# Kernel tuning notes

Hardware: AMD Instinct MI355X
Metric: run time of the kernel (lower is better)

Reference implementation:

```python
import jax, jax.numpy as jnp
import numpy as np

B, N, F, H, N_ITERS = 64, 256, 16, 256, 10


def setup_inputs() -> dict:
    key = jax.random.key(0)
    ks = jax.random.split(key, 20)
    s = 0.05
    jets = jax.random.normal(ks[0], (B, N, F), dtype=jnp.float32)
    # row-normalized dense adjacency (D^-1 A style)
    a = jax.random.uniform(ks[1], (B, N, N), dtype=jnp.float32)
    dads = a / jnp.sum(a, axis=-1, keepdims=True)
    p = lambda k, sh: jax.random.normal(k, sh, dtype=jnp.float32) * s
    return {
        'jets': jets, 'dads': dads,
        'W_emb': p(ks[2], (F, H)), 'b_emb': jnp.zeros((H,), jnp.float32),
        'W_msg': p(ks[3], (H, H)), 'b_msg': jnp.zeros((H,), jnp.float32),
        # GRU vertex update: input = concat(message[H], s[F]) -> H
        'Wz': p(ks[4], (H + F, H)), 'Uz': p(ks[5], (H, H)), 'bz': jnp.zeros((H,), jnp.float32),
        'Wr': p(ks[6], (H + F, H)), 'Ur': p(ks[7], (H, H)), 'br': jnp.zeros((H,), jnp.float32),
        'Wh': p(ks[8], (H + F, H)), 'Uh': p(ks[9], (H, H)), 'bh': jnp.zeros((H,), jnp.float32),
        'W_r1': p(ks[10], (H, H)), 'b_r1': jnp.zeros((H,), jnp.float32),
        'W_r2': p(ks[11], (H, H)), 'b_r2': jnp.zeros((H,), jnp.float32),
    }


def reference(jets, dads, W_emb, b_emb, W_msg, b_msg,
              Wz, Uz, bz, Wr, Ur, br, Wh, Uh, bh,
              W_r1, b_r1, W_r2, b_r2):
    # Embedding: [B,N,F] -> [B,N,H]
    h = jnp.tanh(jets @ W_emb + b_emb)
    for _ in range(N_ITERS):
        # Message: linear then adjacency aggregation + tanh
        m = jnp.tanh(jnp.matmul(dads, h @ W_msg + b_msg))  # [B,N,H]
        # GRU-style vertex update; input = concat(message, original features s)
        x = jnp.concatenate([m, jets], axis=-1)            # [B,N,H+F]
        z = jax.nn.sigmoid(x @ Wz + h @ Uz + bz)
        r = jax.nn.sigmoid(x @ Wr + h @ Ur + br)
        h_tilde = jnp.tanh(x @ Wh + (r * h) @ Uh + bh)
        h = (1.0 - z) * h + z * h_tilde
    # Readout: per-node MLP then sum over nodes -> [B,H]
    out = jnp.sum(jnp.tanh(h @ W_r1 + b_r1) @ W_r2 + b_r2, axis=1)
    return out
```

## Files before the change

kernel.cpp:

```cpp
#include <hip/hip_runtime.h>

#define DEVI __device__ __forceinline__

typedef __attribute__((ext_vector_type(4))) float f32x4;
typedef __attribute__((ext_vector_type(8))) short s16x8;
typedef __attribute__((ext_vector_type(4))) short s16x4;
typedef unsigned short u16;
typedef unsigned int u32;

#define WST 288
#define SROW 264
#define AST 260

DEVI u16 f2bf(float x){
  u32 u = __float_as_uint(x);
  u = (u + 0x7fffu + ((u >> 16) & 1u)) >> 16;
  return (u16)u;
}
DEVI float bf2f(u16 v){ return __uint_as_float(((u32)v) << 16); }

DEVI float fsigm(float x){ return __builtin_amdgcn_rcpf(1.f + __builtin_amdgcn_exp2f(-1.442695041f * x)); }
DEVI float ftanh(float x){ float e = __builtin_amdgcn_exp2f(2.885390082f * x); return 1.f - 2.f * __builtin_amdgcn_rcpf(e + 1.f); }

DEVI s16x8 ld8(const u16* p){ return *(const s16x8*)p; }
DEVI s16x8 ldb64p(const u16* p){
  s16x4 lo = *(const s16x4*)p;
  s16x4 hi = *(const s16x4*)(p + 4);
  s16x8 r;
  r[0]=lo[0]; r[1]=lo[1]; r[2]=lo[2]; r[3]=lo[3];
  r[4]=hi[0]; r[5]=hi[1]; r[6]=hi[2]; r[7]=hi[3];
  return r;
}

DEVI f32x4 ld4bf(const u16* p){
  uint2 v = *(const uint2*)p;
  f32x4 r;
  r[0] = bf2f((u16)(v.x & 0xffff)); r[1] = bf2f((u16)(v.x >> 16));
  r[2] = bf2f((u16)(v.y & 0xffff)); r[3] = bf2f((u16)(v.y >> 16));
  return r;
}

DEVI void st4bf(u16* p, float a, float b, float c, float d){
  uint2 v;
  v.x = (u32)f2bf(a) | ((u32)f2bf(b) << 16);
  v.y = (u32)f2bf(c) | ((u32)f2bf(d) << 16);
  *(uint2*)p = v;
}

#define MFMA(a,b,c) __builtin_amdgcn_mfma_f32_16x16x32_bf16((a),(b),(c),0,0,0)

__global__ void k_prep(
  const float* __restrict__ jets, const float* __restrict__ dads, const float* __restrict__ W_emb,
  const float* __restrict__ W_msg, const float* __restrict__ Wz, const float* __restrict__ Uz,
  const float* __restrict__ Wr, const float* __restrict__ Ur, const float* __restrict__ Wh,
  const float* __restrict__ Uh, const float* __restrict__ W_r1,
  u16* __restrict__ jp, u16* __restrict__ dadsb, u16* __restrict__ Wet, u16* __restrict__ Wmt,
  u16* __restrict__ Wzt, u16* __restrict__ Uzt, u16* __restrict__ Wrt, u16* __restrict__ Urt,
  u16* __restrict__ Wht, u16* __restrict__ Uht, u16* __restrict__ Wr1t)
{
  int blk = blockIdx.x, tid = threadIdx.x;
  if(blk < 1280){
    int mi = blk >> 8, k = blk & 255, j = tid;
    const float* src; u16* dst;
    switch(mi){
      case 0: src = W_msg; dst = Wmt;  break;
      case 1: src = Uz;    dst = Uzt;  break;
      case 2: src = Ur;    dst = Urt;  break;
      case 3: src = Uh;    dst = Uht;  break;
      default: src = W_r1; dst = Wr1t; break;
    }
    dst[j*256 + k] = f2bf(src[k*256 + j]);
  } else if(blk < 2144){
    int q = blk - 1280; int mi = q / 288; int k = q - mi*288; int j = tid;
    const float* src; u16* dst;
    switch(mi){ case 0: src = Wz; dst = Wzt; break; case 1: src = Wr; dst = Wrt; break; default: src = Wh; dst = Wht; break; }
    dst[j*WST + k] = (k < 272) ? f2bf(src[k*256 + j]) : (u16)0;
  } else if(blk < 2176){
    int idx = (blk - 2144)*256 + tid;
    int j = idx >> 5, k = idx & 31;
    Wet[idx] = (k < 16) ? f2bf(W_emb[k*256 + j]) : (u16)0;
  } else if(blk < 4224){
    int idx = (blk - 2176)*256 + tid;
    int n = idx >> 5, k = idx & 31;
    jp[idx] = (k < 16) ? f2bf(jets[n*16 + k]) : (u16)0;
  } else {
    int idx = (blk - 4224)*256 + tid;
    f32x4 v = *(const f32x4*)(dads + (size_t)idx*4);
    st4bf(dadsb + (size_t)idx*4, v[0], v[1], v[2], v[3]);
  }
}

__global__ __launch_bounds__(256,3) void k_embed(
  u16* __restrict__ h, u16* __restrict__ hmo,
  const u16* __restrict__ jp, const u16* __restrict__ Wet, const float* __restrict__ be,
  const u16* __restrict__ Wmt, const float* __restrict__ bm)
{
  __shared__ u16 hbuf[16*SROW];
  const int tid = threadIdx.x;
  const int wv = tid >> 6, lane = tid & 63, ln = lane & 15, qd = lane >> 4;
  const int n0 = blockIdx.x * 16;
  const int b  = n0 >> 8;
  const int nb = n0 & 255;
  const int nodeA = n0 + ln;

  s16x8 jfr = ld8(jp + (size_t)nodeA*32 + qd*8);
#pragma unroll
  for(int t = 0; t < 4; t++){
    int j0 = (wv*4 + t) * 16;
    f32x4 acc = {0.f,0.f,0.f,0.f};
    s16x8 a = ld8(Wet + (size_t)(j0 + ln)*32 + qd*8);
    acc = MFMA(a, jfr, acc);
    f32x4 bv = *(const f32x4*)(be + j0 + qd*4);
    f32x4 hv;
#pragma unroll
    for(int r = 0; r < 4; r++) hv[r] = ftanh(acc[r] + bv[r]);
    st4bf(h + (size_t)nodeA*256 + j0 + qd*4, hv[0], hv[1], hv[2], hv[3]);
    st4bf(&hbuf[ln*SROW + j0 + qd*4], hv[0], hv[1], hv[2], hv[3]);
  }
  __syncthreads();

  s16x8 af[8];
#pragma unroll
  for(int c = 0; c < 8; c++) af[c] = ld8(&hbuf[ln*SROW + c*32 + qd*8]);
#pragma unroll
  for(int tp = 0; tp < 2; tp++){
    int j0 = (wv*4 + tp*2) * 16, j1 = j0 + 16;
    f32x4 a0 = {0.f,0.f,0.f,0.f}, a1 = {0.f,0.f,0.f,0.f};
#pragma unroll
    for(int c = 0; c < 8; c++){
      a0 = MFMA(af[c], ld8(Wmt + (size_t)(j0 + ln)*256 + c*32 + qd*8), a0);
      a1 = MFMA(af[c], ld8(Wmt + (size_t)(j1 + ln)*256 + c*32 + qd*8), a1);
    }
    float b0 = bm[j0 + ln], b1 = bm[j1 + ln];
    st4bf(hmo + (size_t)(b*256 + j0 + ln)*256 + nb + qd*4, a0[0]+b0, a0[1]+b0, a0[2]+b0, a0[3]+b0);
    st4bf(hmo + (size_t)(b*256 + j1 + ln)*256 + nb + qd*4, a1[0]+b1, a1[1]+b1, a1[2]+b1, a1[3]+b1);
  }
}

__global__ __launch_bounds__(256,1) void k_gru(
  u16* __restrict__ h,
  const u16* __restrict__ hmi, u16* __restrict__ hmo,
  const u16* __restrict__ dadsb, const u16* __restrict__ jp,
  const u16* __restrict__ Wzt, const u16* __restrict__ Wrt, const u16* __restrict__ Wht,
  const u16* __restrict__ Uzt, const u16* __restrict__ Urt, const u16* __restrict__ Uht,
  const u16* __restrict__ Wmt,
  const float* __restrict__ bz, const float* __restrict__ br, const float* __restrict__ bhb,
  const float* __restrict__ bm)
{
  __shared__ u16 smM[64*AST];
  __shared__ u16 smB[64*AST];
  const int tid = threadIdx.x;
  const int wv = tid >> 6, lane = tid & 63, ln = lane & 15, qd = lane >> 4;
  const int blk   = blockIdx.x;
  const int batch = (blk & 7) * 8 + (blk >> 5);
  const int group = (blk >> 3) & 3;
  const int n0 = batch * 256 + group * 64;
  const int b  = batch;
  const int nb = group * 64;
  const int j0w = wv * 64;

  const u16* Ab1 = hmi + (size_t)(b*256 + j0w + ln)*256 + qd*8;
  s16x8 Am[3][4];
#pragma unroll
  for(int p = 0; p < 2; p++)
#pragma unroll
    for(int t = 0; t < 4; t++)
      Am[p][t] = ld8(Ab1 + (size_t)t*16*256 + p*32);

  s16x8 jB[4];
#pragma unroll
  for(int i = 0; i < 4; i++) jB[i] = ld8(jp + (size_t)(n0 + i*16 + ln)*32 + qd*8);

  {
    f32x4 acc[4][4];
#pragma unroll
    for(int t = 0; t < 4; t++)
#pragma unroll
      for(int i = 0; i < 4; i++) acc[t][i] = (f32x4){0.f,0.f,0.f,0.f};
    s16x8 Bf[4], Bn[4];
#pragma unroll
    for(int i = 0; i < 4; i++) Bf[i] = ld8(dadsb + (size_t)(n0 + i*16 + ln)*256 + qd*8);
#pragma unroll
    for(int c = 0; c < 8; c++){
      if(c < 6){
#pragma unroll
        for(int t = 0; t < 4; t++) Am[(c+2)%3][t] = ld8(Ab1 + (size_t)t*16*256 + (c+2)*32);
      }
      if(c < 7){
#pragma unroll
        for(int i = 0; i < 4; i++) Bn[i] = ld8(dadsb + (size_t)(n0 + i*16 + ln)*256 + (c+1)*32 + qd*8);
      }
#pragma unroll
      for(int t = 0; t < 4; t++){
        s16x8 A = Am[c%3][t];
#pragma unroll
        for(int i = 0; i < 4; i++) acc[t][i] = MFMA(A, Bf[i], acc[t][i]);
      }
      if(c < 7){
#pragma unroll
        for(int i = 0; i < 4; i++) Bf[i] = Bn[i];
      }
    }
#pragma unroll
    for(int t = 0; t < 4; t++)
#pragma unroll
      for(int i = 0; i < 4; i++)
        st4bf(&smM[(i*16 + ln)*AST + j0w + t*16 + qd*4],
              ftanh(acc[t][i][0]), ftanh(acc[t][i][1]), ftanh(acc[t][i][2]), ftanh(acc[t][i][3]));
  }
  const u16* AbWr = Wrt + (size_t)(j0w + ln)*WST + qd*8;
  const u16* AbUr = Urt + (size_t)(j0w + ln)*256 + qd*8;
  s16x8 RW[3][4], RU[3][4];
#pragma unroll
  for(int p = 0; p < 2; p++)
#pragma unroll
    for(int t = 0; t < 4; t++){
      RW[p][t] = ld8(AbWr + (size_t)t*16*WST + p*32);
      RU[p][t] = ld8(AbUr + (size_t)t*16*256 + p*32);
    }
  __syncthreads();

  {
    f32x4 acc[4][4];
#pragma unroll
    for(int t = 0; t < 4; t++)
#pragma unroll
      for(int i = 0; i < 4; i++) acc[t][i] = (f32x4){0.f,0.f,0.f,0.f};
    s16x8 Ajr[4];
#pragma unroll
    for(int t = 0; t < 4; t++) Ajr[t] = ld8(AbWr + (size_t)t*16*WST + 256);
    s16x8 Bh[4], Bn[4];
#pragma unroll
    for(int i = 0; i < 4; i++) Bh[i] = ld8(h + (size_t)(n0 + i*16 + ln)*256 + qd*8);
#pragma unroll
    for(int c = 0; c < 8; c++){
      if(c < 6){
#pragma unroll
        for(int t = 0; t < 4; t++){
          RW[(c+2)%3][t] = ld8(AbWr + (size_t)t*16*WST + (c+2)*32);
          RU[(c+2)%3][t] = ld8(AbUr + (size_t)t*16*256 + (c+2)*32);
        }
      }
      if(c < 7){
#pragma unroll
        for(int i = 0; i < 4; i++) Bn[i] = ld8(h + (size_t)(n0 + i*16 + ln)*256 + (c+1)*32 + qd*8);
      }
      s16x8 Bm[4];
#pragma unroll
      for(int i = 0; i < 4; i++) Bm[i] = ldb64p(&smM[(i*16 + ln)*AST + c*32 + qd*8]);
#pragma unroll
      for(int t = 0; t < 4; t++){
        s16x8 Aw = RW[c%3][t];
#pragma unroll
        for(int i = 0; i < 4; i++) acc[t][i] = MFMA(Aw, Bm[i], acc[t][i]);
      }
#pragma unroll
      for(int t = 0; t < 4; t++){
        s16x8 Au = RU[c%3][t];
#pragma unroll
        for(int i = 0; i < 4; i++) acc[t][i] = MFMA(Au, Bh[i], acc[t][i]);
      }
      if(c < 7){
#pragma unroll
        for(int i = 0; i < 4; i++) Bh[i] = Bn[i];
      }
    }
#pragma unroll
    for(int t = 0; t < 4; t++)
#pragma unroll
      for(int i = 0; i < 4; i++) acc[t][i] = MFMA(Ajr[t], jB[i], acc[t][i]);
#pragma unroll
    for(int t = 0; t < 4; t++){
      f32x4 bv = *(const f32x4*)(br + j0w + t*16 + qd*4);
#pragma unroll
      for(int i = 0; i < 4; i++){
        f32x4 hv = ld4bf(h + (size_t)(n0 + i*16 + ln)*256 + j0w + t*16 + qd*4);
        st4bf(&smB[(i*16 + ln)*AST + j0w + t*16 + qd*4],
              fsigm(acc[t][i][0]+bv[0])*hv[0], fsigm(acc[t][i][1]+bv[1])*hv[1],
              fsigm(acc[t][i][2]+bv[2])*hv[2], fsigm(acc[t][i][3]+bv[3])*hv[3]);
      }
    }
  }
  const u16* AbWz = Wzt + (size_t)(j0w + ln)*WST + qd*8;
  const u16* AbUz = Uzt + (size_t)(j0w + ln)*256 + qd*8;
  s16x8 ZW[3][4], ZU[3][4];
#pragma unroll
  for(int p = 0; p < 2; p++)
#pragma unroll
    for(int t = 0; t < 4; t++){
      ZW[p][t] = ld8(AbWz + (size_t)t*16*WST + p*32);
      ZU[p][t] = ld8(AbUz + (size_t)t*16*256 + p*32);
    }
  __syncthreads();

  f32x4 zacc[4][4], gacc[4][4];
#pragma unroll
  for(int t = 0; t < 4; t++)
#pragma unroll
    for(int i = 0; i < 4; i++) zacc[t][i] = (f32x4){0.f,0.f,0.f,0.f};
  {
    s16x8 Ajz[4];
#pragma unroll
    for(int t = 0; t < 4; t++) Ajz[t] = ld8(AbWz + (size_t)t*16*WST + 256);
    s16x8 Bh[4], Bn[4];
#pragma unroll
    for(int i = 0; i < 4; i++) Bh[i] = ld8(h + (size_t)(n0 + i*16 + ln)*256 + qd*8);
#pragma unroll
    for(int c = 0; c < 8; c++){
      if(c < 6){
#pragma unroll
        for(int t = 0; t < 4; t++){
          ZW[(c+2)%3][t] = ld8(AbWz + (size_t)t*16*WST + (c+2)*32);
          ZU[(c+2)%3][t] = ld8(AbUz + (size_t)t*16*256 + (c+2)*32);
        }
      }
      if(c < 7){
#pragma unroll
        for(int i = 0; i < 4; i++) Bn[i] = ld8(h + (size_t)(n0 + i*16 + ln)*256 + (c+1)*32 + qd*8);
      }
      s16x8 Bm[4];
#pragma unroll
      for(int i = 0; i < 4; i++) Bm[i] = ldb64p(&smM[(i*16 + ln)*AST + c*32 + qd*8]);
#pragma unroll
      for(int t = 0; t < 4; t++){
        s16x8 Aw = ZW[c%3][t];
#pragma unroll
        for(int i = 0; i < 4; i++) zacc[t][i] = MFMA(Aw, Bm[i], zacc[t][i]);
      }
#pragma unroll
      for(int t = 0; t < 4; t++){
        s16x8 Au = ZU[c%3][t];
#pragma unroll
        for(int i = 0; i < 4; i++) zacc[t][i] = MFMA(Au, Bh[i], zacc[t][i]);
      }
      if(c < 7){
#pragma unroll
        for(int i = 0; i < 4; i++) Bh[i] = Bn[i];
      }
    }
#pragma unroll
    for(int t = 0; t < 4; t++)
#pragma unroll
      for(int i = 0; i < 4; i++) zacc[t][i] = MFMA(Ajz[t], jB[i], zacc[t][i]);
  }

  const u16* AbWh = Wht + (size_t)(j0w + ln)*WST + qd*8;
  const u16* AbUh = Uht + (size_t)(j0w + ln)*256 + qd*8;
  s16x8 GW[3][4], GU[3][4];
#pragma unroll
  for(int p = 0; p < 2; p++)
#pragma unroll
    for(int t = 0; t < 4; t++){
      GW[p][t] = ld8(AbWh + (size_t)t*16*WST + p*32);
      GU[p][t] = ld8(AbUh + (size_t)t*16*256 + p*32);
    }

#pragma unroll
  for(int t = 0; t < 4; t++)
#pragma unroll
    for(int i = 0; i < 4; i++) gacc[t][i] = (f32x4){0.f,0.f,0.f,0.f};
  {
    s16x8 Ajh[4];
#pragma unroll
    for(int t = 0; t < 4; t++) Ajh[t] = ld8(AbWh + (size_t)t*16*WST + 256);
#pragma unroll
    for(int c = 0; c < 8; c++){
      if(c < 6){
#pragma unroll
        for(int t = 0; t < 4; t++){
          GW[(c+2)%3][t] = ld8(AbWh + (size_t)t*16*WST + (c+2)*32);
          GU[(c+2)%3][t] = ld8(AbUh + (size_t)t*16*256 + (c+2)*32);
        }
      }
      s16x8 Bm[4], Brh[4];
#pragma unroll
      for(int i = 0; i < 4; i++){
        Bm[i]  = ldb64p(&smM[(i*16 + ln)*AST + c*32 + qd*8]);
        Brh[i] = ldb64p(&smB[(i*16 + ln)*AST + c*32 + qd*8]);
      }
#pragma unroll
      for(int t = 0; t < 4; t++){
        s16x8 Aw = GW[c%3][t];
#pragma unroll
        for(int i = 0; i < 4; i++) gacc[t][i] = MFMA(Aw, Bm[i], gacc[t][i]);
      }
#pragma unroll
      for(int t = 0; t < 4; t++){
        s16x8 Au = GU[c%3][t];
#pragma unroll
        for(int i = 0; i < 4; i++) gacc[t][i] = MFMA(Au, Brh[i], gacc[t][i]);
      }
    }
#pragma unroll
    for(int t = 0; t < 4; t++)
#pragma unroll
      for(int i = 0; i < 4; i++) gacc[t][i] = MFMA(Ajh[t], jB[i], gacc[t][i]);
  }
  __syncthreads();

#pragma unroll
  for(int t = 0; t < 4; t++){
    f32x4 bzv = *(const f32x4*)(bz + j0w + t*16 + qd*4);
    f32x4 bhv = *(const f32x4*)(bhb + j0w + t*16 + qd*4);
#pragma unroll
    for(int i = 0; i < 4; i++){
      f32x4 hv = ld4bf(h + (size_t)(n0 + i*16 + ln)*256 + j0w + t*16 + qd*4);
      f32x4 hn;
#pragma unroll
      for(int r = 0; r < 4; r++){
        float z  = fsigm(zacc[t][i][r] + bzv[r]);
        float th = ftanh(gacc[t][i][r] + bhv[r]);
        hn[r] = hv[r] + z * (th - hv[r]);
      }
      st4bf(h + (size_t)(n0 + i*16 + ln)*256 + j0w + t*16 + qd*4, hn[0], hn[1], hn[2], hn[3]);
      st4bf(&smM[(i*16 + ln)*AST + j0w + t*16 + qd*4], hn[0], hn[1], hn[2], hn[3]);
    }
  }
  const u16* AbWm = Wmt + (size_t)(j0w + ln)*256 + qd*8;
  s16x8 MW[3][4];
#pragma unroll
  for(int p = 0; p < 2; p++)
#pragma unroll
    for(int t = 0; t < 4; t++)
      MW[p][t] = ld8(AbWm + (size_t)t*16*256 + p*32);
  __syncthreads();

  {
    f32x4 acc[4][4];
#pragma unroll
    for(int t = 0; t < 4; t++)
#pragma unroll
      for(int i = 0; i < 4; i++) acc[t][i] = (f32x4){0.f,0.f,0.f,0.f};
#pragma unroll
    for(int c = 0; c < 8; c++){
      if(c < 6){
#pragma unroll
        for(int t = 0; t < 4; t++) MW[(c+2)%3][t] = ld8(AbWm + (size_t)t*16*256 + (c+2)*32);
      }
      s16x8 Bf[4];
#pragma unroll
      for(int i = 0; i < 4; i++) Bf[i] = ldb64p(&smM[(i*16 + ln)*AST + c*32 + qd*8]);
#pragma unroll
      for(int t = 0; t < 4; t++){
        s16x8 A = MW[c%3][t];
#pragma unroll
        for(int i = 0; i < 4; i++) acc[t][i] = MFMA(A, Bf[i], acc[t][i]);
      }
    }
#pragma unroll
    for(int t = 0; t < 4; t++){
      f32x4 bmv = *(const f32x4*)(bm + j0w + t*16 + qd*4);
#pragma unroll
      for(int i = 0; i < 4; i++){
#pragma unroll
        for(int r = 0; r < 4; r++){
          hmo[(size_t)(b*256 + j0w + t*16 + qd*4 + r)*256 + nb + i*16 + ln] =
            f2bf(acc[t][i][r] + bmv[r]);
        }
      }
    }
  }
}

__global__ __launch_bounds__(256,3) void k_t(
  const u16* __restrict__ h, u16* __restrict__ t_out,
  const u16* __restrict__ Wr1t, const float* __restrict__ br1)
{
  const int tid = threadIdx.x;
  const int wv = tid >> 6, lane = tid & 63, ln = lane & 15, qd = lane >> 4;
  const int n0 = blockIdx.x * 16;
  const int nodeA = n0 + ln;

  s16x8 hfr[8];
#pragma unroll
  for(int c = 0; c < 8; c++) hfr[c] = ld8(h + (size_t)nodeA*256 + c*32 + qd*8);
#pragma unroll
  for(int tp = 0; tp < 2; tp++){
    int j0 = (wv*4 + tp*2) * 16, j1 = j0 + 16;
    f32x4 a0 = {0.f,0.f,0.f,0.f}, a1 = {0.f,0.f,0.f,0.f};
#pragma unroll
    for(int c = 0; c < 8; c++){
      a0 = MFMA(ld8(Wr1t + (size_t)(j0 + ln)*256 + c*32 + qd*8), hfr[c], a0);
      a1 = MFMA(ld8(Wr1t + (size_t)(j1 + ln)*256 + c*32 + qd*8), hfr[c], a1);
    }
    f32x4 b0 = *(const f32x4*)(br1 + j0 + qd*4);
    f32x4 b1 = *(const f32x4*)(br1 + j1 + qd*4);
    st4bf(t_out + (size_t)nodeA*256 + j0 + qd*4,
          ftanh(a0[0]+b0[0]), ftanh(a0[1]+b0[1]), ftanh(a0[2]+b0[2]), ftanh(a0[3]+b0[3]));
    st4bf(t_out + (size_t)nodeA*256 + j1 + qd*4,
          ftanh(a1[0]+b1[0]), ftanh(a1[1]+b1[1]), ftanh(a1[2]+b1[2]), ftanh(a1[3]+b1[3]));
  }
}

__global__ void k_red(const u16* __restrict__ t, const float* __restrict__ W_r2,
                      const float* __restrict__ b_r2, float* __restrict__ out){
  __shared__ float s[256];
  int b = blockIdx.x, k = threadIdx.x;
  float acc = 0.f;
  for(int n = 0; n < 256; n++) acc += bf2f(t[(size_t)(b*256 + n)*256 + k]);
  s[k] = acc;
  __syncthreads();
  int j = threadIdx.x;
  float o = 256.f * b_r2[j];
  for(int k2 = 0; k2 < 256; k2++) o += s[k2] * W_r2[k2*256 + j];
  out[b*256 + j] = o;
}

extern "C" void kernel_launch(void* const* d_in, const int* in_sizes, int n_in,
                              void* d_out, int out_size, void* d_ws, size_t ws_size,
                              hipStream_t stream)
{
  const float* jets  = (const float*)d_in[0];
  const float* dads  = (const float*)d_in[1];
  const float* W_emb = (const float*)d_in[2];
  const float* b_emb = (const float*)d_in[3];
  const float* W_msg = (const float*)d_in[4];
  const float* b_msg = (const float*)d_in[5];
  const float* Wz    = (const float*)d_in[6];
  const float* Uz    = (const float*)d_in[7];
  const float* bz    = (const float*)d_in[8];
  const float* Wr    = (const float*)d_in[9];
  const float* Ur    = (const float*)d_in[10];
  const float* br    = (const float*)d_in[11];
  const float* Wh    = (const float*)d_in[12];
  const float* Uh    = (const float*)d_in[13];
  const float* bh    = (const float*)d_in[14];
  const float* W_r1  = (const float*)d_in[15];
  const float* b_r1  = (const float*)d_in[16];
  const float* W_r2  = (const float*)d_in[17];
  const float* b_r2  = (const float*)d_in[18];

  char* ws = (char*)d_ws;
  u16* h      = (u16*)(ws);
  u16* hmA    = (u16*)(ws + 8388608);
  u16* hmB    = (u16*)(ws + 16777216);
  u16* dadsb  = (u16*)(ws + 25165824);
  u16* jp     = (u16*)(ws + 33554432);
  u16* Wmt    = (u16*)(ws + 34603008);
  u16* Uzt    = (u16*)(ws + 34734080);
  u16* Urt    = (u16*)(ws + 34865152);
  u16* Uht    = (u16*)(ws + 34996224);
  u16* Wr1t   = (u16*)(ws + 35127296);
  u16* Wzt    = (u16*)(ws + 35258368);
  u16* Wrt    = (u16*)(ws + 35405824);
  u16* Wht    = (u16*)(ws + 35553280);
  u16* Wet    = (u16*)(ws + 35700736);
  float* outp = (float*)d_out;

  k_prep<<<8320, 256, 0, stream>>>(jets, dads, W_emb, W_msg, Wz, Uz, Wr, Ur, Wh, Uh, W_r1,
                                   jp, dadsb, Wet, Wmt, Wzt, Uzt, Wrt, Urt, Wht, Uht, Wr1t);
  k_embed<<<1024, 256, 0, stream>>>(h, hmA, jp, Wet, b_emb, Wmt, b_msg);
  for(int it = 0; it < 10; ++it){
    const u16* hin = (it & 1) ? hmB : hmA;
    u16* hout      = (it & 1) ? hmA : hmB;
    k_gru<<<256, 256, 0, stream>>>(h, hin, hout, dadsb, jp,
                                   Wzt, Wrt, Wht, Uzt, Urt, Uht, Wmt,
                                   bz, br, bh, b_msg);
  }
  k_t<<<1024, 256, 0, stream>>>(h, hmB, Wr1t, b_r1);
  k_red<<<64, 256, 0, stream>>>(hmB, W_r2, b_r2, outp);
}
```

Measured before the change: 644.2 us.

## Fuse GRU iterations into persistent cooperative kernel with LDS-resident hidden state

```diff
diff --git a/kernel.cpp b/kernel.cpp
--- a/kernel.cpp
+++ b/kernel.cpp
@@ -1,4 +1,7 @@
 #include <hip/hip_runtime.h>
+#include <hip/hip_cooperative_groups.h>
+
+namespace cg = cooperative_groups;
 
 #define DEVI __device__ __forceinline__
 
@@ -11,6 +14,8 @@
 #define WST 288
 #define SROW 264
 #define AST 260
+
+#define WAITVM(n) __builtin_amdgcn_s_waitcnt(((n)&0xF) | 0x70 | 0xF00 | (((n)>>4)<<14))
 
 DEVI u16 f2bf(float x){
   u32 u = __float_as_uint(x);
@@ -48,6 +53,17 @@
 }
 
 #define MFMA(a,b,c) __builtin_amdgcn_mfma_f32_16x16x32_bf16((a),(b),(c),0,0,0)
+
+DEVI void dma4(const u16* lanebase, int rowStrideElems, int c, u16* ldsbase){
+#pragma unroll
+  for(int q = 0; q < 4; q++){
+    const u16* g = lanebase + (size_t)q*16*rowStrideElems + c*32;
+    __builtin_amdgcn_global_load_lds((__attribute__((address_space(1))) const void*)g,
+                                     (__attribute__((address_space(3))) void*)(ldsbase + q*512),
+                                     16, 0, 0);
+  }
+}
+#define AFRAG(buf, t) ld8(&(buf)[(t)*512 + ln*32 + ((qd ^ ((ln>>1)&3))*8)])
 
 __global__ void k_prep(
   const float* __restrict__ jets, const float* __restrict__ dads, const float* __restrict__ W_emb,
@@ -149,6 +165,7 @@
 {
   __shared__ u16 smM[64*AST];
   __shared__ u16 smB[64*AST];
+  __shared__ __align__(16) u16 stg[4][2][2][2048];
   const int tid = threadIdx.x;
   const int wv = tid >> 6, lane = tid & 63, ln = lane & 15, qd = lane >> 4;
   const int blk   = blockIdx.x;
@@ -159,13 +176,16 @@
   const int nb = group * 64;
   const int j0w = wv * 64;
 
-  const u16* Ab1 = hmi + (size_t)(b*256 + j0w + ln)*256 + qd*8;
-  s16x8 Am[3][4];
-#pragma unroll
-  for(int p = 0; p < 2; p++)
-#pragma unroll
-    for(int t = 0; t < 4; t++)
-      Am[p][t] = ld8(Ab1 + (size_t)t*16*256 + p*32);
+  u16* s0 = &stg[wv][0][0][0];
+  u16* s1 = &stg[wv][1][0][0];
+  u16* u0 = &stg[wv][0][1][0];
+  u16* u1 = &stg[wv][1][1][0];
+
+  const int rw = lane >> 2;
+  const int cs = ((lane & 3) ^ ((lane >> 3) & 3)) * 8;
+
+  const u16* laneA = hmi + (size_t)(b*256 + j0w + rw)*256 + cs;
+  dma4(laneA, 256, 0, s0);
 
   s16x8 jB[4];
 #pragma unroll
@@ -182,17 +202,18 @@
     for(int i = 0; i < 4; i++) Bf[i] = ld8(dadsb + (size_t)(n0 + i*16 + ln)*256 + qd*8);
 #pragma unroll
     for(int c = 0; c < 8; c++){
-      if(c < 6){
-#pragma unroll
-        for(int t = 0; t < 4; t++) Am[(c+2)%3][t] = ld8(Ab1 + (size_t)t*16*256 + (c+2)*32);
-      }
+      u16* cur = (c & 1) ? s1 : s0;
       if(c < 7){
+        dma4(laneA, 256, c+1, (c & 1) ? s0 : s1);
 #pragma unroll
         for(int i = 0; i < 4; i++) Bn[i] = ld8(dadsb + (size_t)(n0 + i*16 + ln)*256 + (c+1)*32 + qd*8);
-      }
-#pragma unroll
-      for(int t = 0; t < 4; t++){
-        s16x8 A = Am[c%3][t];
+        WAITVM(8);
+      } else {
+        WAITVM(0);
+      }
+#pragma unroll
+      for(int t = 0; t < 4; t++){
+        s16x8 A = AFRAG(cur, t);
 #pragma unroll
         for(int i = 0; i < 4; i++) acc[t][i] = MFMA(A, Bf[i], acc[t][i]);
       }
@@ -208,16 +229,10 @@
         st4bf(&smM[(i*16 + ln)*AST + j0w + t*16 + qd*4],
               ftanh(acc[t][i][0]), ftanh(acc[t][i][1]), ftanh(acc[t][i][2]), ftanh(acc[t][i][3]));
   }
-  const u16* AbWr = Wrt + (size_t)(j0w + ln)*WST + qd*8;
-  const u16* AbUr = Urt + (size_t)(j0w + ln)*256 + qd*8;
-  s16x8 RW[3][4], RU[3][4];
-#pragma unroll
-  for(int p = 0; p < 2; p++)
-#pragma unroll
-    for(int t = 0; t < 4; t++){
-      RW[p][t] = ld8(AbWr + (size_t)t*16*WST + p*32);
-      RU[p][t] = ld8(AbUr + (size_t)t*16*256 + p*32);
-    }
+  const u16* laneWr = Wrt + (size_t)(j0w + rw)*WST + cs;
+  const u16* laneUr = Urt + (size_t)(j0w + rw)*256 + cs;
+  dma4(laneWr, WST, 0, s0);
+  dma4(laneUr, 256, 0, u0);
   __syncthreads();
 
   {
@@ -226,37 +241,37 @@
     for(int t = 0; t < 4; t++)
 #pragma unroll
       for(int i = 0; i < 4; i++) acc[t][i] = (f32x4){0.f,0.f,0.f,0.f};
-    s16x8 Ajr[4];
-#pragma unroll
-    for(int t = 0; t < 4; t++) Ajr[t] = ld8(AbWr + (size_t)t*16*WST + 256);
+    s16x8 Aj[4];
+#pragma unroll
+    for(int t = 0; t < 4; t++) Aj[t] = ld8(Wrt + (size_t)(j0w + t*16 + ln)*WST + 256 + qd*8);
     s16x8 Bh[4], Bn[4];
 #pragma unroll
     for(int i = 0; i < 4; i++) Bh[i] = ld8(h + (size_t)(n0 + i*16 + ln)*256 + qd*8);
 #pragma unroll
     for(int c = 0; c < 8; c++){
-      if(c < 6){
-#pragma unroll
-        for(int t = 0; t < 4; t++){
-          RW[(c+2)%3][t] = ld8(AbWr + (size_t)t*16*WST + (c+2)*32);
-          RU[(c+2)%3][t] = ld8(AbUr + (size_t)t*16*256 + (c+2)*32);
-        }
-      }
+      u16* cw = (c & 1) ? s1 : s0;
+      u16* cu = (c & 1) ? u1 : u0;
       if(c < 7){
+        dma4(laneWr, WST, c+1, (c & 1) ? s0 : s1);
+        dma4(laneUr, 256, c+1, (c & 1) ? u0 : u1);
 #pragma unroll
         for(int i = 0; i < 4; i++) Bn[i] = ld8(h + (size_t)(n0 + i*16 + ln)*256 + (c+1)*32 + qd*8);
+        WAITVM(12);
+      } else {
+        WAITVM(0);
       }
       s16x8 Bm[4];
 #pragma unroll
       for(int i = 0; i < 4; i++) Bm[i] = ldb64p(&smM[(i*16 + ln)*AST + c*32 + qd*8]);
 #pragma unroll
       for(int t = 0; t < 4; t++){
-        s16x8 Aw = RW[c%3][t];
+        s16x8 Aw = AFRAG(cw, t);
 #pragma unroll
         for(int i = 0; i < 4; i++) acc[t][i] = MFMA(Aw, Bm[i], acc[t][i]);
       }
 #pragma unroll
       for(int t = 0; t < 4; t++){
-        s16x8 Au = RU[c%3][t];
+        s16x8 Au = AFRAG(cu, t);
 #pragma unroll
         for(int i = 0; i < 4; i++) acc[t][i] = MFMA(Au, Bh[i], acc[t][i]);
       }
@@ -268,7 +283,7 @@
 #pragma unroll
     for(int t = 0; t < 4; t++)
 #pragma unroll
-      for(int i = 0; i < 4; i++) acc[t][i] = MFMA(Ajr[t], jB[i], acc[t][i]);
+      for(int i = 0; i < 4; i++) acc[t][i] = MFMA(Aj[t], jB[i], acc[t][i]);
 #pragma unroll
     for(int t = 0; t < 4; t++){
       f32x4 bv = *(const f32x4*)(br + j0w + t*16 + qd*4);
@@ -281,16 +296,10 @@
       }
     }
   }
-  const u16* AbWz = Wzt + (size_t)(j0w + ln)*WST + qd*8;
-  const u16* AbUz = Uzt + (size_t)(j0w + ln)*256 + qd*8;
-  s16x8 ZW[3][4], ZU[3][4];
-#pragma unroll
-  for(int p = 0; p < 2; p++)
-#pragma unroll
-    for(int t = 0; t < 4; t++){
-      ZW[p][t] = ld8(AbWz + (size_t)t*16*WST + p*32);
-      ZU[p][t] = ld8(AbUz + (size_t)t*16*256 + p*32);
-    }
+  const u16* laneWz = Wzt + (size_t)(j0w + rw)*WST + cs;
+  const u16* laneUz = Uzt + (size_t)(j0w + rw)*256 + cs;
+  dma4(laneWz, WST, 0, s0);
+  dma4(laneUz, 256, 0, u0);
   __syncthreads();
 
   f32x4 zacc[4][4], gacc[4][4];
@@ -299,37 +308,37 @@
 #pragma unroll
     for(int i = 0; i < 4; i++) zacc[t][i] = (f32x4){0.f,0.f,0.f,0.f};
   {
-    s16x8 Ajz[4];
-#pragma unroll
-    for(int t = 0; t < 4; t++) Ajz[t] = ld8(AbWz + (size_t)t*16*WST + 256);
+    s16x8 Aj[4];
+#pragma unroll
+    for(int t = 0; t < 4; t++) Aj[t] = ld8(Wzt + (size_t)(j0w + t*16 + ln)*WST + 256 + qd*8);
     s16x8 Bh[4], Bn[4];
 #pragma unroll
     for(int i = 0; i < 4; i++) Bh[i] = ld8(h + (size_t)(n0 + i*16 + ln)*256 + qd*8);
 #pragma unroll
     for(int c = 0; c < 8; c++){
-      if(c < 6){
-#pragma unroll
-        for(int t = 0; t < 4; t++){
-          ZW[(c+2)%3][t] = ld8(AbWz + (size_t)t*16*WST + (c+2)*32);
-          ZU[(c+2)%3][t] = ld8(AbUz + (size_t)t*16*256 + (c+2)*32);
-        }
-      }
+      u16* cw = (c & 1) ? s1 : s0;
+      u16* cu = (c & 1) ? u1 : u0;
       if(c < 7){
+        dma4(laneWz, WST, c+1, (c & 1) ? s0 : s1);
+        dma4(laneUz, 256, c+1, (c & 1) ? u0 : u1);
 #pragma unroll
         for(int i = 0; i < 4; i++) Bn[i] = ld8(h + (size_t)(n0 + i*16 + ln)*256 + (c+1)*32 + qd*8);
+        WAITVM(12);
+      } else {
+        WAITVM(0);
       }
       s16x8 Bm[4];
 #pragma unroll
       for(int i = 0; i < 4; i++) Bm[i] = ldb64p(&smM[(i*16 + ln)*AST + c*32 + qd*8]);
 #pragma unroll
       for(int t = 0; t < 4; t++){
-        s16x8 Aw = ZW[c%3][t];
+        s16x8 Aw = AFRAG(cw, t);
 #pragma unroll
         for(int i = 0; i < 4; i++) zacc[t][i] = MFMA(Aw, Bm[i], zacc[t][i]);
       }
 #pragma unroll
       for(int t = 0; t < 4; t++){
-        s16x8 Au = ZU[c%3][t];
+        s16x8 Au = AFRAG(cu, t);
 #pragma unroll
         for(int i = 0; i < 4; i++) zacc[t][i] = MFMA(Au, Bh[i], zacc[t][i]);
       }
@@ -341,36 +350,32 @@
 #pragma unroll
     for(int t = 0; t < 4; t++)
 #pragma unroll
-      for(int i = 0; i < 4; i++) zacc[t][i] = MFMA(Ajz[t], jB[i], zacc[t][i]);
-  }
-
-  const u16* AbWh = Wht + (size_t)(j0w + ln)*WST + qd*8;
-  const u16* AbUh = Uht + (size_t)(j0w + ln)*256 + qd*8;
-  s16x8 GW[3][4], GU[3][4];
-#pragma unroll
-  for(int p = 0; p < 2; p++)
-#pragma unroll
-    for(int t = 0; t < 4; t++){
-      GW[p][t] = ld8(AbWh + (size_t)t*16*WST + p*32);
-      GU[p][t] = ld8(AbUh + (size_t)t*16*256 + p*32);
-    }
+      for(int i = 0; i < 4; i++) zacc[t][i] = MFMA(Aj[t], jB[i], zacc[t][i]);
+  }
+
+  const u16* laneWh = Wht + (size_t)(j0w + rw)*WST + cs;
+  const u16* laneUh = Uht + (size_t)(j0w + rw)*256 + cs;
+  dma4(laneWh, WST, 0, s0);
+  dma4(laneUh, 256, 0, u0);
 
 #pragma unroll
   for(int t = 0; t < 4; t++)
 #pragma unroll
     for(int i = 0; i < 4; i++) gacc[t][i] = (f32x4){0.f,0.f,0.f,0.f};
   {
-    s16x8 Ajh[4];
-#pragma unroll
-    for(int t = 0; t < 4; t++) Ajh[t] = ld8(AbWh + (size_t)t*16*WST + 256);
+    s16x8 Aj[4];
+#pragma unroll
+    for(int t = 0; t < 4; t++) Aj[t] = ld8(Wht + (size_t)(j0w + t*16 + ln)*WST + 256 + qd*8);
 #pragma unroll
     for(int c = 0; c < 8; c++){
-      if(c < 6){
-#pragma unroll
-        for(int t = 0; t < 4; t++){
-          GW[(c+2)%3][t] = ld8(AbWh + (size_t)t*16*WST + (c+2)*32);
-          GU[(c+2)%3][t] = ld8(AbUh + (size_t)t*16*256 + (c+2)*32);
-        }
+      u16* cw = (c & 1) ? s1 : s0;
+      u16* cu = (c & 1) ? u1 : u0;
+      if(c < 7){
+        dma4(laneWh, WST, c+1, (c & 1) ? s0 : s1);
+        dma4(laneUh, 256, c+1, (c & 1) ? u0 : u1);
+        WAITVM(8);
+      } else {
+        WAITVM(0);
       }
       s16x8 Bm[4], Brh[4];
 #pragma unroll
@@ -380,13 +385,13 @@
       }
 #pragma unroll
       for(int t = 0; t < 4; t++){
-        s16x8 Aw = GW[c%3][t];
+        s16x8 Aw = AFRAG(cw, t);
 #pragma unroll
         for(int i = 0; i < 4; i++) gacc[t][i] = MFMA(Aw, Bm[i], gacc[t][i]);
       }
 #pragma unroll
       for(int t = 0; t < 4; t++){
-        s16x8 Au = GU[c%3][t];
+        s16x8 Au = AFRAG(cu, t);
 #pragma unroll
         for(int i = 0; i < 4; i++) gacc[t][i] = MFMA(Au, Brh[i], gacc[t][i]);
       }
@@ -394,7 +399,7 @@
 #pragma unroll
     for(int t = 0; t < 4; t++)
 #pragma unroll
-      for(int i = 0; i < 4; i++) gacc[t][i] = MFMA(Ajh[t], jB[i], gacc[t][i]);
+      for(int i = 0; i < 4; i++) gacc[t][i] = MFMA(Aj[t], jB[i], gacc[t][i]);
   }
   __syncthreads();
 
@@ -416,13 +421,8 @@
       st4bf(&smM[(i*16 + ln)*AST + j0w + t*16 + qd*4], hn[0], hn[1], hn[2], hn[3]);
     }
   }
-  const u16* AbWm = Wmt + (size_t)(j0w + ln)*256 + qd*8;
-  s16x8 MW[3][4];
-#pragma unroll
-  for(int p = 0; p < 2; p++)
-#pragma unroll
-    for(int t = 0; t < 4; t++)
-      MW[p][t] = ld8(AbWm + (size_t)t*16*256 + p*32);
+  const u16* laneWm = Wmt + (size_t)(j0w + rw)*256 + cs;
+  dma4(laneWm, 256, 0, s0);
   __syncthreads();
 
   {
@@ -433,16 +433,19 @@
       for(int i = 0; i < 4; i++) acc[t][i] = (f32x4){0.f,0.f,0.f,0.f};
 #pragma unroll
     for(int c = 0; c < 8; c++){
-      if(c < 6){
-#pragma unroll
-        for(int t = 0; t < 4; t++) MW[(c+2)%3][t] = ld8(AbWm + (size_t)t*16*256 + (c+2)*32);
+      u16* cur = (c & 1) ? s1 : s0;
+      if(c < 7){
+        dma4(laneWm, 256, c+1, (c & 1) ? s0 : s1);
+        WAITVM(4);
+      } else {
+        WAITVM(0);
       }
       s16x8 Bf[4];
 #pragma unroll
       for(int i = 0; i < 4; i++) Bf[i] = ldb64p(&smM[(i*16 + ln)*AST + c*32 + qd*8]);
 #pragma unroll
       for(int t = 0; t < 4; t++){
-        s16x8 A = MW[c%3][t];
+        s16x8 A = AFRAG(cur, t);
 #pragma unroll
         for(int i = 0; i < 4; i++) acc[t][i] = MFMA(A, Bf[i], acc[t][i]);
       }
@@ -460,6 +463,341 @@
       }
     }
   }
+}
+
+__global__ __launch_bounds__(256,1) void k_gru_persist(
+  u16* __restrict__ h,
+  u16* __restrict__ hmA, u16* __restrict__ hmB,
+  const u16* __restrict__ dadsb, const u16* __restrict__ jp,
+  const u16* __restrict__ Wzt, const u16* __restrict__ Wrt, const u16* __restrict__ Wht,
+  const u16* __restrict__ Uzt, const u16* __restrict__ Urt, const u16* __restrict__ Uht,
+  const u16* __restrict__ Wmt,
+  const float* __restrict__ bz, const float* __restrict__ br, const float* __restrict__ bhb,
+  const float* __restrict__ bm)
+{
+  cg::grid_group grid = cg::this_grid();
+  __shared__ u16 smM[64*AST];
+  __shared__ u16 smB[64*AST];
+  __shared__ u16 hL[64*AST];
+  const int tid = threadIdx.x;
+  const int wv = tid >> 6, lane = tid & 63, ln = lane & 15, qd = lane >> 4;
+  const int blk   = blockIdx.x;
+  const int batch = (blk & 7) * 8 + (blk >> 5);
+  const int group = (blk >> 3) & 3;
+  const int n0 = batch * 256 + group * 64;
+  const int b  = batch;
+  const int nb = group * 64;
+  const int j0w = wv * 64;
+
+#pragma unroll
+  for(int t = 0; t < 4; t++)
+#pragma unroll
+    for(int i = 0; i < 4; i++)
+      *(uint2*)&hL[(i*16 + ln)*AST + j0w + t*16 + qd*4] =
+        *(const uint2*)&h[(size_t)(n0 + i*16 + ln)*256 + j0w + t*16 + qd*4];
+
+  s16x8 jB[4];
+#pragma unroll
+  for(int i = 0; i < 4; i++) jB[i] = ld8(jp + (size_t)(n0 + i*16 + ln)*32 + qd*8);
+
+  const u16* AbWr = Wrt + (size_t)(j0w + ln)*WST + qd*8;
+  const u16* AbUr = Urt + (size_t)(j0w + ln)*256 + qd*8;
+  const u16* AbWz = Wzt + (size_t)(j0w + ln)*WST + qd*8;
+  const u16* AbUz = Uzt + (size_t)(j0w + ln)*256 + qd*8;
+  const u16* AbWh = Wht + (size_t)(j0w + ln)*WST + qd*8;
+  const u16* AbUh = Uht + (size_t)(j0w + ln)*256 + qd*8;
+  const u16* AbWm = Wmt + (size_t)(j0w + ln)*256 + qd*8;
+
+  for(int it = 0; it < 10; ++it){
+    const u16* hmi = (it & 1) ? hmB : hmA;
+    u16*       hmo = (it & 1) ? hmA : hmB;
+
+    const u16* Ab1 = hmi + (size_t)(b*256 + j0w + ln)*256 + qd*8;
+    s16x8 Am[3][4];
+#pragma unroll
+    for(int p = 0; p < 2; p++)
+#pragma unroll
+      for(int t = 0; t < 4; t++)
+        Am[p][t] = ld8(Ab1 + (size_t)t*16*256 + p*32);
+    {
+      f32x4 acc[4][4];
+#pragma unroll
+      for(int t = 0; t < 4; t++)
+#pragma unroll
+        for(int i = 0; i < 4; i++) acc[t][i] = (f32x4){0.f,0.f,0.f,0.f};
+      s16x8 Bf[4], Bn[4];
+#pragma unroll
+      for(int i = 0; i < 4; i++) Bf[i] = ld8(dadsb + (size_t)(n0 + i*16 + ln)*256 + qd*8);
+#pragma unroll
+      for(int c = 0; c < 8; c++){
+        if(c < 6){
+#pragma unroll
+          for(int t = 0; t < 4; t++) Am[(c+2)%3][t] = ld8(Ab1 + (size_t)t*16*256 + (c+2)*32);
+        }
+        if(c < 7){
+#pragma unroll
+          for(int i = 0; i < 4; i++) Bn[i] = ld8(dadsb + (size_t)(n0 + i*16 + ln)*256 + (c+1)*32 + qd*8);
+        }
+#pragma unroll
+        for(int t = 0; t < 4; t++){
+          s16x8 A = Am[c%3][t];
+#pragma unroll
+          for(int i = 0; i < 4; i++) acc[t][i] = MFMA(A, Bf[i], acc[t][i]);
+        }
+        if(c < 7){
+#pragma unroll
+          for(int i = 0; i < 4; i++) Bf[i] = Bn[i];
+        }
+      }
+#pragma unroll
+      for(int t = 0; t < 4; t++)
+#pragma unroll
+        for(int i = 0; i < 4; i++)
+          st4bf(&smM[(i*16 + ln)*AST + j0w + t*16 + qd*4],
+                ftanh(acc[t][i][0]), ftanh(acc[t][i][1]), ftanh(acc[t][i][2]), ftanh(acc[t][i][3]));
+    }
+    s16x8 RW[3][4], RU[3][4];
+#pragma unroll
+    for(int p = 0; p < 2; p++)
+#pragma unroll
+      for(int t = 0; t < 4; t++){
+        RW[p][t] = ld8(AbWr + (size_t)t*16*WST + p*32);
+        RU[p][t] = ld8(AbUr + (size_t)t*16*256 + p*32);
+      }
+    __syncthreads();
+
+    {
+      f32x4 acc[4][4];
+#pragma unroll
+      for(int t = 0; t < 4; t++)
+#pragma unroll
+        for(int i = 0; i < 4; i++) acc[t][i] = (f32x4){0.f,0.f,0.f,0.f};
+      s16x8 Ajr[4];
+#pragma unroll
+      for(int t = 0; t < 4; t++) Ajr[t] = ld8(AbWr + (size_t)t*16*WST + 256);
+#pragma unroll
+      for(int c = 0; c < 8; c++){
+        if(c < 6){
+#pragma unroll
+          for(int t = 0; t < 4; t++){
+            RW[(c+2)%3][t] = ld8(AbWr + (size_t)t*16*WST + (c+2)*32);
+            RU[(c+2)%3][t] = ld8(AbUr + (size_t)t*16*256 + (c+2)*32);
+          }
+        }
+        s16x8 Bm[4], Bh[4];
+#pragma unroll
+        for(int i = 0; i < 4; i++){
+          Bm[i] = ldb64p(&smM[(i*16 + ln)*AST + c*32 + qd*8]);
+          Bh[i] = ldb64p(&hL [(i*16 + ln)*AST + c*32 + qd*8]);
+        }
+#pragma unroll
+        for(int t = 0; t < 4; t++){
+          s16x8 Aw = RW[c%3][t];
+#pragma unroll
+          for(int i = 0; i < 4; i++) acc[t][i] = MFMA(Aw, Bm[i], acc[t][i]);
+        }
+#pragma unroll
+        for(int t = 0; t < 4; t++){
+          s16x8 Au = RU[c%3][t];
+#pragma unroll
+          for(int i = 0; i < 4; i++) acc[t][i] = MFMA(Au, Bh[i], acc[t][i]);
+        }
+      }
+#pragma unroll
+      for(int t = 0; t < 4; t++)
+#pragma unroll
+        for(int i = 0; i < 4; i++) acc[t][i] = MFMA(Ajr[t], jB[i], acc[t][i]);
+#pragma unroll
+      for(int t = 0; t < 4; t++){
+        f32x4 bv = *(const f32x4*)(br + j0w + t*16 + qd*4);
+#pragma unroll
+        for(int i = 0; i < 4; i++){
+          f32x4 hv = ld4bf(&hL[(i*16 + ln)*AST + j0w + t*16 + qd*4]);
+          st4bf(&smB[(i*16 + ln)*AST + j0w + t*16 + qd*4],
+                fsigm(acc[t][i][0]+bv[0])*hv[0], fsigm(acc[t][i][1]+bv[1])*hv[1],
+                fsigm(acc[t][i][2]+bv[2])*hv[2], fsigm(acc[t][i][3]+bv[3])*hv[3]);
+        }
+      }
+    }
+    s16x8 ZW[3][4], ZU[3][4];
+#pragma unroll
+    for(int p = 0; p < 2; p++)
+#pragma unroll
+      for(int t = 0; t < 4; t++){
+        ZW[p][t] = ld8(AbWz + (size_t)t*16*WST + p*32);
+        ZU[p][t] = ld8(AbUz + (size_t)t*16*256 + p*32);
+      }
+    __syncthreads();
+
+    f32x4 zacc[4][4], gacc[4][4];
+#pragma unroll
+    for(int t = 0; t < 4; t++)
+#pragma unroll
+      for(int i = 0; i < 4; i++) zacc[t][i] = (f32x4){0.f,0.f,0.f,0.f};
+    {
+      s16x8 Ajz[4];
+#pragma unroll
+      for(int t = 0; t < 4; t++) Ajz[t] = ld8(AbWz + (size_t)t*16*WST + 256);
+#pragma unroll
+      for(int c = 0; c < 8; c++){
+        if(c < 6){
+#pragma unroll
+          for(int t = 0; t < 4; t++){
+            ZW[(c+2)%3][t] = ld8(AbWz + (size_t)t*16*WST + (c+2)*32);
+            ZU[(c+2)%3][t] = ld8(AbUz + (size_t)t*16*256 + (c+2)*32);
+          }
+        }
+        s16x8 Bm[4], Bh[4];
+#pragma unroll
+        for(int i = 0; i < 4; i++){
+          Bm[i] = ldb64p(&smM[(i*16 + ln)*AST + c*32 + qd*8]);
+          Bh[i] = ldb64p(&hL [(i*16 + ln)*AST + c*32 + qd*8]);
+        }
+#pragma unroll
+        for(int t = 0; t < 4; t++){
+          s16x8 Aw = ZW[c%3][t];
+#pragma unroll
+          for(int i = 0; i < 4; i++) zacc[t][i] = MFMA(Aw, Bm[i], zacc[t][i]);
+        }
+#pragma unroll
+        for(int t = 0; t < 4; t++){
+          s16x8 Au = ZU[c%3][t];
+#pragma unroll
+          for(int i = 0; i < 4; i++) zacc[t][i] = MFMA(Au, Bh[i], zacc[t][i]);
+        }
+      }
+#pragma unroll
+      for(int t = 0; t < 4; t++)
+#pragma unroll
+        for(int i = 0; i < 4; i++) zacc[t][i] = MFMA(Ajz[t], jB[i], zacc[t][i]);
+    }
+
+    s16x8 GW[3][4], GU[3][4];
+#pragma unroll
+    for(int p = 0; p < 2; p++)
+#pragma unroll
+      for(int t = 0; t < 4; t++){
+        GW[p][t] = ld8(AbWh + (size_t)t*16*WST + p*32);
+        GU[p][t] = ld8(AbUh + (size_t)t*16*256 + p*32);
+      }
+
+#pragma unroll
+    for(int t = 0; t < 4; t++)
+#pragma unroll
+      for(int i = 0; i < 4; i++) gacc[t][i] = (f32x4){0.f,0.f,0.f,0.f};
+    {
+      s16x8 Ajh[4];
+#pragma unroll
+      for(int t = 0; t < 4; t++) Ajh[t] = ld8(AbWh + (size_t)t*16*WST + 256);
+#pragma unroll
+      for(int c = 0; c < 8; c++){
+        if(c < 6){
+#pragma unroll
+          for(int t = 0; t < 4; t++){
+            GW[(c+2)%3][t] = ld8(AbWh + (size_t)t*16*WST + (c+2)*32);
+            GU[(c+2)%3][t] = ld8(AbUh + (size_t)t*16*256 + (c+2)*32);
+          }
+        }
+        s16x8 Bm[4], Brh[4];
+#pragma unroll
+        for(int i = 0; i < 4; i++){
+          Bm[i]  = ldb64p(&smM[(i*16 + ln)*AST + c*32 + qd*8]);
+          Brh[i] = ldb64p(&smB[(i*16 + ln)*AST + c*32 + qd*8]);
+        }
+#pragma unroll
+        for(int t = 0; t < 4; t++){
+          s16x8 Aw = GW[c%3][t];
+#pragma unroll
+          for(int i = 0; i < 4; i++) gacc[t][i] = MFMA(Aw, Bm[i], gacc[t][i]);
+        }
+#pragma unroll
+        for(int t = 0; t < 4; t++){
+          s16x8 Au = GU[c%3][t];
+#pragma unroll
+          for(int i = 0; i < 4; i++) gacc[t][i] = MFMA(Au, Brh[i], gacc[t][i]);
+        }
+      }
+#pragma unroll
+      for(int t = 0; t < 4; t++)
+#pragma unroll
+        for(int i = 0; i < 4; i++) gacc[t][i] = MFMA(Ajh[t], jB[i], gacc[t][i]);
+    }
+    __syncthreads();
+
+#pragma unroll
+    for(int t = 0; t < 4; t++){
+      f32x4 bzv = *(const f32x4*)(bz + j0w + t*16 + qd*4);
+      f32x4 bhv = *(const f32x4*)(bhb + j0w + t*16 + qd*4);
+#pragma unroll
+      for(int i = 0; i < 4; i++){
+        f32x4 hv = ld4bf(&hL[(i*16 + ln)*AST + j0w + t*16 + qd*4]);
+        f32x4 hn;
+#pragma unroll
+        for(int r = 0; r < 4; r++){
+          float z  = fsigm(zacc[t][i][r] + bzv[r]);
+          float th = ftanh(gacc[t][i][r] + bhv[r]);
+          hn[r] = hv[r] + z * (th - hv[r]);
+        }
+        st4bf(&hL [(i*16 + ln)*AST + j0w + t*16 + qd*4], hn[0], hn[1], hn[2], hn[3]);
+        st4bf(&smM[(i*16 + ln)*AST + j0w + t*16 + qd*4], hn[0], hn[1], hn[2], hn[3]);
+      }
+    }
+    if(it == 9) break;
+
+    s16x8 MW[3][4];
+#pragma unroll
+    for(int p = 0; p < 2; p++)
+#pragma unroll
+      for(int t = 0; t < 4; t++)
+        MW[p][t] = ld8(AbWm + (size_t)t*16*256 + p*32);
+    __syncthreads();
+
+    {
+      f32x4 acc[4][4];
+#pragma unroll
+      for(int t = 0; t < 4; t++)
+#pragma unroll
+        for(int i = 0; i < 4; i++) acc[t][i] = (f32x4){0.f,0.f,0.f,0.f};
+#pragma unroll
+      for(int c = 0; c < 8; c++){
+        if(c < 6){
+#pragma unroll
+          for(int t = 0; t < 4; t++) MW[(c+2)%3][t] = ld8(AbWm + (size_t)t*16*256 + (c+2)*32);
+        }
+        s16x8 Bf[4];
+#pragma unroll
+        for(int i = 0; i < 4; i++) Bf[i] = ldb64p(&smM[(i*16 + ln)*AST + c*32 + qd*8]);
+#pragma unroll
+        for(int t = 0; t < 4; t++){
+          s16x8 A = MW[c%3][t];
+#pragma unroll
+          for(int i = 0; i < 4; i++) acc[t][i] = MFMA(A, Bf[i], acc[t][i]);
+        }
+      }
+#pragma unroll
+      for(int t = 0; t < 4; t++){
+        f32x4 bmv = *(const f32x4*)(bm + j0w + t*16 + qd*4);
+#pragma unroll
+        for(int i = 0; i < 4; i++){
+#pragma unroll
+          for(int r = 0; r < 4; r++){
+            hmo[(size_t)(b*256 + j0w + t*16 + qd*4 + r)*256 + nb + i*16 + ln] =
+              f2bf(acc[t][i][r] + bmv[r]);
+          }
+        }
+      }
+    }
+    __threadfence();
+    grid.sync();
+    __threadfence();
+  }
+
+#pragma unroll
+  for(int t = 0; t < 4; t++)
+#pragma unroll
+    for(int i = 0; i < 4; i++)
+      *(uint2*)&h[(size_t)(n0 + i*16 + ln)*256 + j0w + t*16 + qd*4] =
+        *(const uint2*)&hL[(i*16 + ln)*AST + j0w + t*16 + qd*4];
 }
 
 __global__ __launch_bounds__(256,3) void k_t(
@@ -550,13 +888,27 @@
   k_prep<<<8320, 256, 0, stream>>>(jets, dads, W_emb, W_msg, Wz, Uz, Wr, Ur, Wh, Uh, W_r1,
                                    jp, dadsb, Wet, Wmt, Wzt, Uzt, Wrt, Urt, Wht, Uht, Wr1t);
   k_embed<<<1024, 256, 0, stream>>>(h, hmA, jp, Wet, b_emb, Wmt, b_msg);
-  for(int it = 0; it < 10; ++it){
-    const u16* hin = (it & 1) ? hmB : hmA;
-    u16* hout      = (it & 1) ? hmA : hmB;
-    k_gru<<<256, 256, 0, stream>>>(h, hin, hout, dadsb, jp,
-                                   Wzt, Wrt, Wht, Uzt, Urt, Uht, Wmt,
-                                   bz, br, bh, b_msg);
-  }
+
+  {
+    void* args[16] = {
+      (void*)&h, (void*)&hmA, (void*)&hmB, (void*)&dadsb, (void*)&jp,
+      (void*)&Wzt, (void*)&Wrt, (void*)&Wht,
+      (void*)&Uzt, (void*)&Urt, (void*)&Uht, (void*)&Wmt,
+      (void*)&bz, (void*)&br, (void*)&bh, (void*)&b_msg
+    };
+    hipError_t e = hipLaunchCooperativeKernel((const void*)k_gru_persist,
+                                              dim3(256), dim3(256), args, 0, stream);
+    if(e != hipSuccess){
+      for(int it = 0; it < 10; ++it){
+        const u16* hin = (it & 1) ? hmB : hmA;
+        u16* hout      = (it & 1) ? hmA : hmB;
+        k_gru<<<256, 256, 0, stream>>>(h, hin, hout, dadsb, jp,
+                                       Wzt, Wrt, Wht, Uzt, Urt, Uht, Wmt,
+                                       bz, br, bh, b_msg);
+      }
+    }
+  }
+
   k_t<<<1024, 256, 0, stream>>>(h, hmB, Wr1t, b_r1);
   k_red<<<64, 256, 0, stream>>>(hmB, W_r2, b_r2, outp);
 }
```

Result: slower. 1.749 ms (+171.5%).
